# Performance work log

Hardware: AMD Instinct MI355X
Metric: run time of the kernel (lower is better)

Reference implementation:

```python
import jax, jax.numpy as jnp
import numpy as np

N = 100000   # nodes
E = 640000   # edges
G = 256      # graphs in batch
L = 3        # mpnn layers
D_IN = 64    # in_node_channels
E_IN = 16    # in_edge_channels
H = 128      # hidden width (uniform)


def setup_inputs() -> dict:
    key = jax.random.key(0)
    ks = jax.random.split(key, 20)
    s = 0.05
    inp = {
        "x": jax.random.normal(ks[0], (N, D_IN), dtype=jnp.float32),
        "edge_index": jax.random.randint(ks[1], (2, E), 0, N, dtype=jnp.int64),
        "edge_attr": jax.random.normal(ks[2], (E, E_IN), dtype=jnp.float32),
        "batch_vec": jnp.sort(jax.random.randint(ks[3], (N,), 0, G, dtype=jnp.int64)),
        # input encoders
        "Wn0": jax.random.normal(ks[4], (D_IN, H), dtype=jnp.float32) * s,
        "bn0": jnp.zeros((H,), jnp.float32),
        "We0": jax.random.normal(ks[5], (E_IN, H), dtype=jnp.float32) * s,
        "be0": jnp.zeros((H,), jnp.float32),
        # per-layer MPNN params (stacked over L)
        "WM": jax.random.normal(ks[6], (L, 3 * H, H), dtype=jnp.float32) * s,
        "bM": jnp.zeros((L, H), jnp.float32),
        "WU": jax.random.normal(ks[7], (L, 2 * H, H), dtype=jnp.float32) * s,
        "bU": jnp.zeros((L, H), jnp.float32),
        # per-layer node/edge linear layers
        "Wn": jax.random.normal(ks[8], (L, H, H), dtype=jnp.float32) * s,
        "bn": jnp.zeros((L, H), jnp.float32),
        "We": jax.random.normal(ks[9], (L, H, H), dtype=jnp.float32) * s,
        "be": jnp.zeros((L, H), jnp.float32),
        "Wh": jax.random.normal(ks[10], (H, 1), dtype=jnp.float32) * s,
        "bh": jnp.zeros((1,), jnp.float32),
    }
    return inp


def _mpnn_layer(x, edge_attr, src, dst, WM, bM, WU, bU):
    # message: relu(Linear([x_i, x_j, e]))  (x_i = target, x_j = source)
    xi = x[dst]                                   # [E, H]
    xj = x[src]                                   # [E, H]
    m = jax.nn.relu(jnp.concatenate([xi, xj, edge_attr], axis=-1) @ WM + bM)
    # mean aggregation at target nodes
    agg = jax.ops.segment_sum(m, dst, num_segments=N)        # [N, H]
    cnt = jax.ops.segment_sum(jnp.ones((m.shape[0], 1), x.dtype), dst,
                              num_segments=N)
    agg = agg / jnp.maximum(cnt, 1.0)
    # update: relu(Linear([x, aggr_out]))
    return jax.nn.relu(jnp.concatenate([x, agg], axis=-1) @ WU + bU)


def reference(x, edge_index, edge_attr, batch_vec,
              Wn0, bn0, We0, be0, WM, bM, WU, bU, Wn, bn, We, be, Wh, bh):
    src, dst = edge_index[0], edge_index[1]       # PyG source_to_target flow
    h = jax.nn.relu(x @ Wn0 + bn0)                # NodeFeatureLinear
    e = jax.nn.relu(edge_attr @ We0 + be0)        # EdgeFeatureLinear
    for i in range(L):
        h = _mpnn_layer(h, e, src, dst, WM[i], bM[i], WU[i], bU[i])
        h = jax.nn.relu(h @ Wn[i] + bn[i])
        e = jax.nn.relu(e @ We[i] + be[i])
    # global mean pool over graphs
    sums = jax.ops.segment_sum(h, batch_vec, num_segments=G)  # [G, H]
    cnts = jax.ops.segment_sum(jnp.ones((N, 1), h.dtype), batch_vec,
                               num_segments=G)
    pooled = sums / jnp.maximum(cnts, 1.0)
    return pooled @ Wh + bh                       # [G, 1]
```

## Files before the change

### kernel.cpp

```cpp
#include <hip/hip_runtime.h>

#define NN 100000
#define EE 640000
#define GG 256
#define LL 3
#define HH 128

constexpr int BM = 64;
constexpr int BK = 16;

typedef _Float16 f16;
typedef f16 f16x8 __attribute__((ext_vector_type(8)));
typedef f16 f16x4 __attribute__((ext_vector_type(4)));
typedef f16 f16x2 __attribute__((ext_vector_type(2)));
typedef float f32x4 __attribute__((ext_vector_type(4)));

#define TSTR 136

__device__ __forceinline__ void gload_lds16(const void* g, void* l) {
  __builtin_amdgcn_global_load_lds(
      (const __attribute__((address_space(1))) void*)g,
      (__attribute__((address_space(3))) void*)l, 16, 0, 0);
}

__global__ void prep_w(const float* __restrict__ We0,
                       const float* __restrict__ We,
                       const float* __restrict__ WM,
                       const float* __restrict__ Wn0,
                       const float* __restrict__ Wn,
                       const float* __restrict__ WU, f16* __restrict__ out) {
  const int buf = blockIdx.x >> 3;
  const int rowg = blockIdx.x & 7;
  const float* src;
  int K;
  if (buf == 0) {
    src = We0; K = 16;
  } else if (buf <= 2) {
    src = We + (size_t)(buf - 1) * HH * HH; K = HH;
  } else if (buf <= 5) {
    src = WM + (size_t)(buf - 3) * 3 * HH * HH + 2 * HH * HH; K = HH;
  } else if (buf == 6) {
    src = Wn0; K = 64;
  } else if (buf <= 9) {
    src = WM + (size_t)(buf - 7) * 3 * HH * HH; K = HH;
  } else if (buf <= 12) {
    src = WM + (size_t)(buf - 10) * 3 * HH * HH + HH * HH; K = HH;
  } else if (buf <= 15) {
    src = Wn + (size_t)(buf - 13) * HH * HH; K = HH;
  } else {
    const int t = buf - 16;
    src = WU + (size_t)(t >> 1) * 2 * HH * HH + (size_t)(t & 1) * HH * HH;
    K = HH;
  }
  f16* dst = out + (size_t)buf * HH * TSTR;
  for (int idx = threadIdx.x; idx < 16 * TSTR; idx += 256) {
    const int n = rowg * 16 + idx / TSTR;
    const int k = idx % TSTR;
    const float v = (k < K) ? src[(size_t)k * HH + n] : 0.f;
    dst[(size_t)n * TSTR + k] = (f16)v;
  }
}

struct GemmCtx {
  f16* Xs; f16* Wt; float* V;
  int tid, lane, wv, l15, q, m0;
};

__device__ __forceinline__ void ctx_init(GemmCtx& c, char* smem) {
  c.Xs = (f16*)smem;
  c.Wt = (f16*)(smem + 17408);
  c.V = (float*)(smem + 17408);
  c.tid = threadIdx.x;
  c.lane = c.tid & 63;
  c.wv = c.tid >> 6;
  c.l15 = c.lane & 15;
  c.q = c.lane >> 4;
  c.m0 = blockIdx.x * 64;
}

__device__ __forceinline__ void c_stageW(GemmCtx& c, const f16* Wg) {
  const char* g = (const char*)Wg;
  char* l = (char*)c.Wt;
#pragma unroll
  for (int i = 0; i < 8; ++i)
    gload_lds16(g + c.tid * 16 + i * 4096, l + c.tid * 16 + i * 4096);
  if (c.tid < 128) gload_lds16(g + c.tid * 16 + 32768, l + c.tid * 16 + 32768);
}

__device__ __forceinline__ void c_stageXf32(GemmCtx& c, const float* Xp,
                                            int stride, int KC, bool scale,
                                            const float* inv, int M) {
  const int npr = KC >> 2;
  for (int i = c.tid; i < 64 * npr; i += 256) {
    const int row = i / npr;
    const int c4 = (i - row * npr) << 2;
    float4 v = make_float4(0.f, 0.f, 0.f, 0.f);
    if (c.m0 + row < M) {
      v = *(const float4*)(Xp + (size_t)(c.m0 + row) * stride + c4);
      if (scale) {
        const float s = inv[c.m0 + row];
        v.x *= s; v.y *= s; v.z *= s; v.w *= s;
      }
    }
    f16x4 hv;
    hv[0] = (f16)v.x; hv[1] = (f16)v.y; hv[2] = (f16)v.z; hv[3] = (f16)v.w;
    *(f16x4*)&c.Xs[(size_t)row * TSTR + c4] = hv;
  }
}

__device__ __forceinline__ void c_stageX16(GemmCtx& c, const f16* Xp, int M) {
  for (int i = c.tid; i < 1024; i += 256) {
    const int row = i >> 4;
    const int c8 = (i & 15) << 3;
    f16x8 v = {};
    if (c.m0 + row < M) v = *(const f16x8*)(Xp + (size_t)(c.m0 + row) * HH + c8);
    *(f16x8*)&c.Xs[(size_t)row * TSTR + c8] = v;
  }
}

__device__ __forceinline__ void c_mfmaN(GemmCtx& c, f32x4 (&ac)[4][2],
                                        int nk) {
  for (int kk = 0; kk < nk; ++kk) {
    f16x8 a[4], b[2];
#pragma unroll
    for (int mi = 0; mi < 4; ++mi)
      a[mi] = *(const f16x8*)&c.Xs[(size_t)(mi * 16 + c.l15) * TSTR + kk * 32 +
                                   c.q * 8];
#pragma unroll
    for (int ni = 0; ni < 2; ++ni)
      b[ni] = *(const f16x8*)&c.Wt[(size_t)((c.wv * 2 + ni) * 16 + c.l15) *
                                       TSTR +
                                   kk * 32 + c.q * 8];
#pragma unroll
    for (int mi = 0; mi < 4; ++mi)
#pragma unroll
      for (int ni = 0; ni < 2; ++ni)
        ac[mi][ni] = __builtin_amdgcn_mfma_f32_16x16x32_f16(a[mi], b[ni],
                                                            ac[mi][ni], 0, 0,
                                                            0);
  }
}

__device__ __forceinline__ void c_zero(f32x4 (&ac)[4][2]) {
#pragma unroll
  for (int mi = 0; mi < 4; ++mi)
#pragma unroll
    for (int ni = 0; ni < 2; ++ni) {
      f32x4 z = {};
      ac[mi][ni] = z;
    }
}

__device__ __forceinline__ void c_reluXs(GemmCtx& c, f32x4 (&ac)[4][2],
                                         const float* bias) {
  const float bv0 = bias[c.wv * 32 + c.l15];
  const float bv1 = bias[c.wv * 32 + 16 + c.l15];
#pragma unroll
  for (int mi = 0; mi < 4; ++mi)
#pragma unroll
    for (int ni = 0; ni < 2; ++ni) {
      const float bb = ni ? bv1 : bv0;
#pragma unroll
      for (int rr = 0; rr < 4; ++rr) {
        float v = ac[mi][ni][rr] + bb;
        v = v > 0.f ? v : 0.f;
        c.Xs[(size_t)(mi * 16 + c.q * 4 + rr) * TSTR + c.wv * 32 + ni * 16 +
             c.l15] = (f16)v;
      }
    }
}

__device__ __forceinline__ void c_dumpV(GemmCtx& c, f32x4 (&ac)[4][2]) {
#pragma unroll
  for (int mi = 0; mi < 4; ++mi)
#pragma unroll
    for (int ni = 0; ni < 2; ++ni)
#pragma unroll
      for (int rr = 0; rr < 4; ++rr)
        c.V[(size_t)(mi * 16 + c.q * 4 + rr) * 132 + c.wv * 32 + ni * 16 +
            c.l15] = ac[mi][ni][rr];
}

__device__ __forceinline__ void c_storeV16(GemmCtx& c, f16* op, int M) {
  const int tm = (c.tid >> 4) << 2;
  const int tn = (c.tid & 15) << 3;
#pragma unroll
  for (int i = 0; i < 4; ++i) {
    const int r = c.m0 + tm + i;
    if (r >= M) continue;
    const float* vp = &c.V[(size_t)(tm + i) * 132 + tn];
    f16x8 hv;
#pragma unroll
    for (int j = 0; j < 8; ++j) hv[j] = (f16)vp[j];
    *(f16x8*)(op + (size_t)r * HH + tn) = hv;
  }
}

__device__ __forceinline__ void c_storeXs16(GemmCtx& c, f16* op, int M) {
  const int tm = (c.tid >> 4) << 2;
  const int tn = (c.tid & 15) << 3;
#pragma unroll
  for (int i = 0; i < 4; ++i) {
    const int r = c.m0 + tm + i;
    if (r >= M) continue;
    *(f16x8*)(op + (size_t)r * HH + tn) =
        *(const f16x8*)&c.Xs[(size_t)(tm + i) * TSTR + tn];
  }
}

__device__ __forceinline__ void c_projAB(GemmCtx& c, f32x4 (&ac)[4][2],
                                         const f16* WA, const f16* WBp,
                                         f16* A16, f16* B16, int M) {
  c_zero(ac);
  c_mfmaN(c, ac, 4);
  __syncthreads();
  c_dumpV(c, ac);
  __syncthreads();
  c_storeV16(c, A16, M);
  __syncthreads();
  c_stageW(c, WBp);
  __syncthreads();
  c_zero(ac);
  c_mfmaN(c, ac, 4);
  __syncthreads();
  c_dumpV(c, ac);
  __syncthreads();
  c_storeV16(c, B16, M);
}

__global__ __launch_bounds__(256) void fused_enc(
    const float* __restrict__ x, const f16* __restrict__ Wn0T,
    const float* __restrict__ bn0, f16* __restrict__ h16,
    const f16* __restrict__ WA, const f16* __restrict__ WBp,
    f16* __restrict__ A16, f16* __restrict__ B16, int M) {
  __shared__ __align__(16) char smem[17408 + 34816];
  GemmCtx c; ctx_init(c, smem);
  f32x4 acc[4][2];
  c_zero(acc);
  c_stageW(c, Wn0T);
  c_stageXf32(c, x, 64, 64, false, nullptr, M);
  __syncthreads();
  c_mfmaN(c, acc, 2);
  __syncthreads();
  c_reluXs(c, acc, bn0);
  c_stageW(c, WA);
  __syncthreads();
  c_storeXs16(c, h16, M);
  c_projAB(c, acc, WA, WBp, A16, B16, M);
}

template <int HAS_AB>
__global__ __launch_bounds__(256) void fused_upd(
    const f16* __restrict__ h, const f16* __restrict__ WU01,
    const float* __restrict__ bU, const float* __restrict__ agg,
    const float* __restrict__ invc, const f16* __restrict__ WnT,
    const float* __restrict__ bn, const f16* __restrict__ WA,
    const f16* __restrict__ WBp, f16* __restrict__ hout,
    f16* __restrict__ A16, f16* __restrict__ B16, int M) {
  __shared__ __align__(16) char smem[17408 + 34816];
  GemmCtx c; ctx_init(c, smem);
  f32x4 acc[4][2];
  c_zero(acc);
  c_stageW(c, WU01);
  c_stageX16(c, h, M);
  __syncthreads();
  c_mfmaN(c, acc, 4);
  __syncthreads();
  c_stageW(c, WU01 + (size_t)HH * TSTR);
  c_stageXf32(c, agg, HH, 128, true, invc, M);
  __syncthreads();
  c_mfmaN(c, acc, 4);
  __syncthreads();
  c_reluXs(c, acc, bU);
  c_stageW(c, WnT);
  __syncthreads();
  c_zero(acc);
  c_mfmaN(c, acc, 4);
  __syncthreads();
  c_reluXs(c, acc, bn);
  if (HAS_AB) c_stageW(c, WA);
  __syncthreads();
  c_storeXs16(c, hout, M);
  if (HAS_AB) c_projAB(c, acc, WA, WBp, A16, B16, M);
}

template <int CHAIN>
__global__ __launch_bounds__(512) void msg_k(
    const float* __restrict__ ea, const f16* __restrict__ W0T,
    const float* __restrict__ be0, const f16* __restrict__ WeT,
    const float* __restrict__ beL, const f16* __restrict__ WMeT,
    const float* __restrict__ bMl, const f16* __restrict__ A,
    const f16* __restrict__ B, const int* __restrict__ sIdx,
    const int* __restrict__ sSrc, const int* __restrict__ sDst,
    float* __restrict__ agg) {
  __shared__ __align__(16) char smem[34816 + 34816 + 512];
  f16* Tc = (f16*)smem;
  f16* Wc = (f16*)(smem + 34816);
  float* V = (float*)smem;
  int* dstS = (int*)(smem + 69632);

  const int tid = threadIdx.x;
  const int lane = tid & 63;
  const int wv = tid >> 6;
  const int ew = (wv >> 2) * 64;
  const int wn = wv & 3;
  const int l15 = lane & 15;
  const int q = lane >> 4;
  const int r0 = blockIdx.x * 128;

  auto wptr = [&](int p) -> const f16* {
    if (p == 0) return W0T;
    if (p <= CHAIN) return WeT + (size_t)(p - 1) * HH * TSTR;
    return WMeT;
  };

  auto stage_w = [&](const f16* Wg) {
    const char* g = (const char*)Wg;
    char* l = (char*)Wc;
#pragma unroll
    for (int i = 0; i < 4; ++i)
      gload_lds16(g + tid * 16 + i * 8192, l + tid * 16 + i * 8192);
    if (tid < 128) gload_lds16(g + tid * 16 + 32768, l + tid * 16 + 32768);
  };

  stage_w(wptr(0));
  {
    const int xr = tid >> 2;
    const int xc = (tid & 3) << 2;
    const int e = sIdx[r0 + xr];
    const float4 v = *(const float4*)(ea + (size_t)e * 16 + xc);
    f16x4 hv;
    hv[0] = (f16)v.x; hv[1] = (f16)v.y; hv[2] = (f16)v.z; hv[3] = (f16)v.w;
    *(f16x4*)&Tc[(size_t)xr * TSTR + xc] = hv;
    f16x4 z = {};
    *(f16x4*)&Tc[(size_t)xr * TSTR + 16 + xc] = z;
    if (tid < 128) dstS[tid] = sDst[r0 + tid];
  }

  f32x4 acc[4][2];

  auto zero_acc = [&]() {
#pragma unroll
    for (int mi = 0; mi < 4; ++mi)
#pragma unroll
      for (int ni = 0; ni < 2; ++ni) {
        f32x4 z = {};
        acc[mi][ni] = z;
      }
  };

  auto mfma_steps = [&](int nk) {
    for (int kk = 0; kk < nk; ++kk) {
      f16x8 a[4], b[2];
#pragma unroll
      for (int mi = 0; mi < 4; ++mi)
        a[mi] = *(const f16x8*)&Tc[(size_t)(ew + mi * 16 + l15) * TSTR +
                                   kk * 32 + q * 8];
#pragma unroll
      for (int ni = 0; ni < 2; ++ni)
        b[ni] = *(const f16x8*)&Wc[(size_t)((wn * 2 + ni) * 16 + l15) * TSTR +
                                   kk * 32 + q * 8];
#pragma unroll
      for (int mi = 0; mi < 4; ++mi)
#pragma unroll
        for (int ni = 0; ni < 2; ++ni)
          acc[mi][ni] = __builtin_amdgcn_mfma_f32_16x16x32_f16(
              a[mi], b[ni], acc[mi][ni], 0, 0, 0);
    }
  };

  auto relu_body = [&](const float* bias) {
    float bv0 = bias[wn * 32 + l15];
    float bv1 = bias[wn * 32 + 16 + l15];
#pragma unroll
    for (int mi = 0; mi < 4; ++mi)
#pragma unroll
      for (int ni = 0; ni < 2; ++ni) {
        const float bb = ni ? bv1 : bv0;
#pragma unroll
        for (int rr = 0; rr < 4; ++rr) {
          float v = acc[mi][ni][rr] + bb;
          v = v > 0.f ? v : 0.f;
          Tc[(size_t)(ew + mi * 16 + q * 4 + rr) * TSTR + wn * 32 + ni * 16 +
             l15] = (f16)v;
        }
      }
  };

  zero_acc();
  __syncthreads();
  mfma_steps(1);
  __syncthreads();
  stage_w(wptr(1));
  relu_body(be0);
  __syncthreads();

#pragma unroll
  for (int s = 0; s < CHAIN; ++s) {
    zero_acc();
    mfma_steps(4);
    __syncthreads();
    stage_w(wptr(s + 2));
    relu_body(beL + (size_t)s * HH);
    __syncthreads();
  }

  zero_acc();
  mfma_steps(4);
  __syncthreads();

#pragma unroll
  for (int mi = 0; mi < 4; ++mi)
#pragma unroll
    for (int ni = 0; ni < 2; ++ni)
#pragma unroll
      for (int rr = 0; rr < 4; ++rr)
        V[(size_t)(ew + mi * 16 + q * 4 + rr) * 129 + wn * 32 + ni * 16 +
          l15] = acc[mi][ni][rr];
  __syncthreads();

  const int tm = (tid >> 4) << 2;
  const int tn = (tid & 15) << 3;
  const float4 m0v = *(const float4*)(bMl + tn);
  const float4 m1v = *(const float4*)(bMl + tn + 4);
  const float mv[8] = {m0v.x, m0v.y, m0v.z, m0v.w,
                       m1v.x, m1v.y, m1v.z, m1v.w};
#pragma unroll
  for (int i = 0; i < 4; ++i) {
    const int rr = r0 + tm + i;
    const int d = dstS[tm + i];
    const int s = sSrc[rr];
    const f16x8 a8 = *(const f16x8*)(A + (size_t)d * HH + tn);
    const f16x8 b8 = *(const f16x8*)(B + (size_t)s * HH + tn);
    float* vp = &V[(size_t)(tm + i) * 129 + tn];
#pragma unroll
    for (int j = 0; j < 8; ++j)
      vp[j] = fmaxf(vp[j] + (float)a8[j] + (float)b8[j] + mv[j], 0.f);
  }
  __syncthreads();

  const int c = tid & 127;
  const int h = tid >> 7;
  float racc = 0.f;
  int cur = dstS[h * 32];
  bool first = true;
  for (int e2 = h * 32; e2 < h * 32 + 32; ++e2) {
    const int d = dstS[e2];
    if (d != cur) {
      if (first) {
        atomicAdd(&agg[(size_t)cur * HH + c], racc);
        first = false;
      } else {
        agg[(size_t)cur * HH + c] = racc;
      }
      racc = 0.f;
      cur = d;
    }
    racc += V[(size_t)e2 * 129 + c];
  }
  atomicAdd(&agg[(size_t)cur * HH + c], racc);
}

__global__ void count_kernel(const int* __restrict__ dst, int* cnt, int E) {
  const int i = blockIdx.x * 256 + threadIdx.x;
  if (i < E) atomicAdd(&cnt[dst[i]], 1);
}

__global__ void invcnt_kernel(const int* __restrict__ cnt, float* inv, int n) {
  const int i = blockIdx.x * 256 + threadIdx.x;
  if (i < n) inv[i] = 1.0f / (float)max(cnt[i], 1);
}

__global__ void scan_block(const int* __restrict__ cnt, int* excl, int* bsum,
                           int n) {
  __shared__ int s[256];
  const int tx = threadIdx.x;
  const int i = blockIdx.x * 256 + tx;
  const int v = (i < n) ? cnt[i] : 0;
  s[tx] = v;
  __syncthreads();
  for (int off = 1; off < 256; off <<= 1) {
    int tv = (tx >= off) ? s[tx - off] : 0;
    __syncthreads();
    s[tx] += tv;
    __syncthreads();
  }
  if (i < n) excl[i] = s[tx] - v;
  if (tx == 255) bsum[blockIdx.x] = s[255];
}

__global__ __launch_bounds__(512) void scan_bsum(int* bsum, int nb) {
  __shared__ int s[512];
  const int t = threadIdx.x;
  const int v0 = (t < nb) ? bsum[t] : 0;
  s[t] = v0;
  __syncthreads();
  for (int off = 1; off < 512; off <<= 1) {
    const int tv = (t >= off) ? s[t - off] : 0;
    __syncthreads();
    s[t] += tv;
    __syncthreads();
  }
  if (t < nb) bsum[t] = s[t] - v0;
}

__global__ void scan_add(int* excl, const int* __restrict__ bsum, int n) {
  const int i = blockIdx.x * 256 + threadIdx.x;
  if (i < n) excl[i] += bsum[blockIdx.x];
}

__global__ void scatter_edges(const int* __restrict__ dst,
                              const int* __restrict__ src,
                              const int* __restrict__ off, int* ctr, int* sIdx,
                              int* sSrc, int* sDst, int E) {
  const int e = blockIdx.x * 256 + threadIdx.x;
  if (e >= E) return;
  const int d = dst[e];
  const int p = off[d] + atomicAdd(&ctr[d], 1);
  sIdx[p] = e;
  sSrc[p] = src[e];
  sDst[p] = d;
}

__global__ void pool_accum(const f16* __restrict__ h,
                           const int* __restrict__ batch,
                           float* __restrict__ gsum, int M) {
  const int col = threadIdx.x;
  const int r0 = blockIdx.x * 64;
  const int rend = min(r0 + 64, M);
  if (r0 >= M) return;
  float acc = 0.f;
  int cur = batch[r0];
  for (int r = r0; r < rend; ++r) {
    const int b = batch[r];
    if (b != cur) {
      atomicAdd(&gsum[(size_t)cur * HH + col], acc);
      acc = 0.f;
      cur = b;
    }
    acc += (float)h[(size_t)r * HH + col];
  }
  atomicAdd(&gsum[(size_t)cur * HH + col], acc);
}

__global__ void gcnt_kernel(const int* __restrict__ batch, int* gcnt, int n) {
  const int i = blockIdx.x * 256 + threadIdx.x;
  if (i < n) atomicAdd(&gcnt[batch[i]], 1);
}

__global__ void head_kernel(const float* __restrict__ gsum,
                            const int* __restrict__ gcnt,
                            const float* __restrict__ Wh,
                            const float* __restrict__ bh,
                            float* __restrict__ out) {
  const int g = blockIdx.x;
  const int t = threadIdx.x;
  float v = gsum[(size_t)g * HH + t] * Wh[t];
#pragma unroll
  for (int o = 32; o > 0; o >>= 1) v += __shfl_down(v, o, 64);
  __shared__ float red[2];
  if ((t & 63) == 0) red[t >> 6] = v;
  __syncthreads();
  if (t == 0) {
    const float s = red[0] + red[1];
    const float c = (float)max(gcnt[g], 1);
    out[g] = s / c + bh[0];
  }
}

extern "C" void kernel_launch(void* const* d_in, const int* in_sizes, int n_in,
                              void* d_out, int out_size, void* d_ws,
                              size_t ws_size, hipStream_t stream) {
  (void)in_sizes; (void)n_in; (void)out_size;
  const float* x = (const float*)d_in[0];
  const int* ei = (const int*)d_in[1];
  const float* ea = (const float*)d_in[2];
  const int* batch = (const int*)d_in[3];
  const float* Wn0 = (const float*)d_in[4];
  const float* bn0 = (const float*)d_in[5];
  const float* We0 = (const float*)d_in[6];
  const float* be0 = (const float*)d_in[7];
  const float* WM = (const float*)d_in[8];
  const float* bM = (const float*)d_in[9];
  const float* WU = (const float*)d_in[10];
  const float* bU = (const float*)d_in[11];
  const float* Wn = (const float*)d_in[12];
  const float* bn = (const float*)d_in[13];
  const float* We = (const float*)d_in[14];
  const float* be = (const float*)d_in[15];
  const float* Wh = (const float*)d_in[16];
  const float* bh = (const float*)d_in[17];

  const int* srcI = ei;
  const int* dstI = ei + EE;

  float* w = (float*)d_ws;
  size_t o = 0;
  f16* h16 = (f16*)(w + o);  o += (size_t)NN * HH / 2;
  float* agg = w + o;  o += (size_t)NN * HH;
  f16* A16 = (f16*)(w + o); o += (size_t)NN * HH / 2;
  f16* B16 = (f16*)(w + o); o += (size_t)NN * HH / 2;
  float* gsum = w + o; o += (size_t)GG * HH;
  float* invc = w + o; o += (size_t)NN;
  int* cnt = (int*)(w + o);  o += (size_t)NN;
  int* gcnt = (int*)(w + o); o += (size_t)GG;
  int* off = (int*)(w + o);  o += (size_t)NN;
  int* ctr = (int*)(w + o);  o += (size_t)NN;
  int* bsum = (int*)(w + o); o += 512;
  int* sIdx = (int*)(w + o); o += (size_t)EE;
  int* sSrc = (int*)(w + o); o += (size_t)EE;
  int* sDst = (int*)(w + o); o += (size_t)EE;
  f16* Wp = (f16*)(w + o);   o += (size_t)22 * HH * TSTR / 2;
  if (o * sizeof(float) > ws_size) return;

  auto WB = [&](int i) { return Wp + (size_t)i * HH * TSTR; };

  const dim3 blk(256);
  const int gridN = (NN + BM - 1) / BM;
  const int gridE = EE / 128;
  const int NBLK = (NN + 255) / 256;

  hipMemsetAsync(cnt, 0, (size_t)NN * sizeof(int), stream);
  hipMemsetAsync(ctr, 0, (size_t)NN * sizeof(int), stream);
  hipMemsetAsync(gsum, 0, (size_t)GG * HH * sizeof(float), stream);
  hipMemsetAsync(gcnt, 0, (size_t)GG * sizeof(int), stream);

  count_kernel<<<(EE + 255) / 256, blk, 0, stream>>>(dstI, cnt, EE);
  scan_block<<<NBLK, blk, 0, stream>>>(cnt, off, bsum, NN);
  scan_bsum<<<1, dim3(512), 0, stream>>>(bsum, NBLK);
  scan_add<<<NBLK, blk, 0, stream>>>(off, bsum, NN);
  scatter_edges<<<(EE + 255) / 256, blk, 0, stream>>>(dstI, srcI, off, ctr,
                                                      sIdx, sSrc, sDst, EE);
  invcnt_kernel<<<(NN + 255) / 256, blk, 0, stream>>>(cnt, invc, NN);
  prep_w<<<22 * 8, blk, 0, stream>>>(We0, We, WM, Wn0, Wn, WU, Wp);

  fused_enc<<<gridN, blk, 0, stream>>>(x, WB(6), bn0, h16, WB(7), WB(10),
                                       A16, B16, NN);

  for (int l = 0; l < LL; ++l) {
    hipMemsetAsync(agg, 0, (size_t)NN * HH * sizeof(float), stream);
    switch (l) {
      case 0:
        msg_k<0><<<gridE, dim3(512), 0, stream>>>(
            ea, WB(0), be0, WB(1), be, WB(3), bM + 0 * HH, A16, B16, sIdx,
            sSrc, sDst, agg);
        break;
      case 1:
        msg_k<1><<<gridE, dim3(512), 0, stream>>>(
            ea, WB(0), be0, WB(1), be, WB(4), bM + 1 * HH, A16, B16, sIdx,
            sSrc, sDst, agg);
        break;
      default:
        msg_k<2><<<gridE, dim3(512), 0, stream>>>(
            ea, WB(0), be0, WB(1), be, WB(5), bM + 2 * HH, A16, B16, sIdx,
            sSrc, sDst, agg);
        break;
    }
    if (l < LL - 1) {
      fused_upd<1><<<gridN, blk, 0, stream>>>(
          h16, WB(16 + 2 * l), bU + l * HH, agg, invc, WB(13 + l), bn + l * HH,
          WB(7 + l + 1), WB(10 + l + 1), h16, A16, B16, NN);
    } else {
      fused_upd<0><<<gridN, blk, 0, stream>>>(
          h16, WB(16 + 2 * l), bU + l * HH, agg, invc, WB(13 + l), bn + l * HH,
          nullptr, nullptr, h16, nullptr, nullptr, NN);
    }
  }

  pool_accum<<<gridN, dim3(128), 0, stream>>>(h16, batch, gsum, NN);
  gcnt_kernel<<<(NN + 255) / 256, blk, 0, stream>>>(batch, gcnt, NN);
  head_kernel<<<GG, dim3(128), 0, stream>>>(gsum, gcnt, Wh, bh, (float*)d_out);
}
```

Baseline: 985.2 us.

## Fuse pooling into last update, shrink message kernel to 256 threads with f16 staging

The final update kernel now accumulates the global mean-pool sums directly from its LDS tile, so the separate pool_accum and gcnt kernels go away. gcnt counting moves into count_kernel and the inverse-count computation into scan_add, which removes two more launches. The message kernel now runs 256 threads per block, each wave covering a 64x64 output tile with 16 accumulators. Its message buffer is staged as f16 instead of f32, halving LDS traffic at the cost of extra rounding before aggregation, and the larger per-wave tile raises register pressure.

```diff
diff --git a/kernel.cpp b/kernel.cpp
--- a/kernel.cpp
+++ b/kernel.cpp
@@ -7,7 +7,6 @@
 #define HH 128
 
 constexpr int BM = 64;
-constexpr int BK = 16;
 
 typedef _Float16 f16;
 typedef f16 f16x8 __attribute__((ext_vector_type(8)));
@@ -256,9 +255,13 @@
     const float* __restrict__ invc, const f16* __restrict__ WnT,
     const float* __restrict__ bn, const f16* __restrict__ WA,
     const f16* __restrict__ WBp, f16* __restrict__ hout,
-    f16* __restrict__ A16, f16* __restrict__ B16, int M) {
+    f16* __restrict__ A16, f16* __restrict__ B16,
+    const int* __restrict__ batch, float* __restrict__ gsum, int M) {
   __shared__ __align__(16) char smem[17408 + 34816];
+  __shared__ int bat[64];
   GemmCtx c; ctx_init(c, smem);
+  if (!HAS_AB && c.tid < 64 && c.m0 + c.tid < M)
+    bat[c.tid] = batch[c.m0 + c.tid];
   f32x4 acc[4][2];
   c_zero(acc);
   c_stageW(c, WU01);
@@ -280,12 +283,33 @@
   c_reluXs(c, acc, bn);
   if (HAS_AB) c_stageW(c, WA);
   __syncthreads();
-  c_storeXs16(c, hout, M);
-  if (HAS_AB) c_projAB(c, acc, WA, WBp, A16, B16, M);
+  if (HAS_AB) {
+    c_storeXs16(c, hout, M);
+    c_projAB(c, acc, WA, WBp, A16, B16, M);
+  } else {
+    const int col = c.tid & 127;
+    const int rg = c.tid >> 7;
+    const int lo = rg * 32;
+    const int hi = min(lo + 32, M - c.m0);
+    if (lo < hi) {
+      float a2 = 0.f;
+      int cur = bat[lo];
+      for (int r = lo; r < hi; ++r) {
+        const int b = bat[r];
+        if (b != cur) {
+          atomicAdd(&gsum[(size_t)cur * HH + col], a2);
+          a2 = 0.f;
+          cur = b;
+        }
+        a2 += (float)c.Xs[(size_t)r * TSTR + col];
+      }
+      atomicAdd(&gsum[(size_t)cur * HH + col], a2);
+    }
+  }
 }
 
 template <int CHAIN>
-__global__ __launch_bounds__(512) void msg_k(
+__global__ __launch_bounds__(256) void msg_k(
     const float* __restrict__ ea, const f16* __restrict__ W0T,
     const float* __restrict__ be0, const f16* __restrict__ WeT,
     const float* __restrict__ beL, const f16* __restrict__ WMeT,
@@ -296,14 +320,14 @@
   __shared__ __align__(16) char smem[34816 + 34816 + 512];
   f16* Tc = (f16*)smem;
   f16* Wc = (f16*)(smem + 34816);
-  float* V = (float*)smem;
+  f16* V16 = (f16*)smem;
   int* dstS = (int*)(smem + 69632);
 
   const int tid = threadIdx.x;
   const int lane = tid & 63;
   const int wv = tid >> 6;
-  const int ew = (wv >> 2) * 64;
-  const int wn = wv & 3;
+  const int eh = (wv >> 1) * 64;
+  const int ch = wv & 1;
   const int l15 = lane & 15;
   const int q = lane >> 4;
   const int r0 = blockIdx.x * 128;
@@ -318,32 +342,34 @@
     const char* g = (const char*)Wg;
     char* l = (char*)Wc;
 #pragma unroll
-    for (int i = 0; i < 4; ++i)
-      gload_lds16(g + tid * 16 + i * 8192, l + tid * 16 + i * 8192);
+    for (int i = 0; i < 8; ++i)
+      gload_lds16(g + tid * 16 + i * 4096, l + tid * 16 + i * 4096);
     if (tid < 128) gload_lds16(g + tid * 16 + 32768, l + tid * 16 + 32768);
   };
 
   stage_w(wptr(0));
   {
-    const int xr = tid >> 2;
-    const int xc = (tid & 3) << 2;
+    const int xr = tid >> 1;
+    const int hf = (tid & 1) << 3;
     const int e = sIdx[r0 + xr];
-    const float4 v = *(const float4*)(ea + (size_t)e * 16 + xc);
-    f16x4 hv;
-    hv[0] = (f16)v.x; hv[1] = (f16)v.y; hv[2] = (f16)v.z; hv[3] = (f16)v.w;
-    *(f16x4*)&Tc[(size_t)xr * TSTR + xc] = hv;
-    f16x4 z = {};
-    *(f16x4*)&Tc[(size_t)xr * TSTR + 16 + xc] = z;
+    const float4 v0 = *(const float4*)(ea + (size_t)e * 16 + hf);
+    const float4 v1 = *(const float4*)(ea + (size_t)e * 16 + hf + 4);
+    f16x8 hv;
+    hv[0] = (f16)v0.x; hv[1] = (f16)v0.y; hv[2] = (f16)v0.z; hv[3] = (f16)v0.w;
+    hv[4] = (f16)v1.x; hv[5] = (f16)v1.y; hv[6] = (f16)v1.z; hv[7] = (f16)v1.w;
+    *(f16x8*)&Tc[(size_t)xr * TSTR + hf] = hv;
+    f16x8 z = {};
+    *(f16x8*)&Tc[(size_t)xr * TSTR + 16 + hf] = z;
     if (tid < 128) dstS[tid] = sDst[r0 + tid];
   }
 
-  f32x4 acc[4][2];
+  f32x4 acc[4][4];
 
   auto zero_acc = [&]() {
 #pragma unroll
     for (int mi = 0; mi < 4; ++mi)
 #pragma unroll
-      for (int ni = 0; ni < 2; ++ni) {
+      for (int ni = 0; ni < 4; ++ni) {
         f32x4 z = {};
         acc[mi][ni] = z;
       }
@@ -351,37 +377,35 @@
 
   auto mfma_steps = [&](int nk) {
     for (int kk = 0; kk < nk; ++kk) {
-      f16x8 a[4], b[2];
+      f16x8 a[4], b[4];
 #pragma unroll
       for (int mi = 0; mi < 4; ++mi)
-        a[mi] = *(const f16x8*)&Tc[(size_t)(ew + mi * 16 + l15) * TSTR +
+        a[mi] = *(const f16x8*)&Tc[(size_t)(eh + mi * 16 + l15) * TSTR +
                                    kk * 32 + q * 8];
 #pragma unroll
-      for (int ni = 0; ni < 2; ++ni)
-        b[ni] = *(const f16x8*)&Wc[(size_t)((wn * 2 + ni) * 16 + l15) * TSTR +
+      for (int ni = 0; ni < 4; ++ni)
+        b[ni] = *(const f16x8*)&Wc[(size_t)((ch * 4 + ni) * 16 + l15) * TSTR +
                                    kk * 32 + q * 8];
 #pragma unroll
       for (int mi = 0; mi < 4; ++mi)
 #pragma unroll
-        for (int ni = 0; ni < 2; ++ni)
+        for (int ni = 0; ni < 4; ++ni)
           acc[mi][ni] = __builtin_amdgcn_mfma_f32_16x16x32_f16(
               a[mi], b[ni], acc[mi][ni], 0, 0, 0);
     }
   };
 
   auto relu_body = [&](const float* bias) {
-    float bv0 = bias[wn * 32 + l15];
-    float bv1 = bias[wn * 32 + 16 + l15];
 #pragma unroll
     for (int mi = 0; mi < 4; ++mi)
 #pragma unroll
-      for (int ni = 0; ni < 2; ++ni) {
-        const float bb = ni ? bv1 : bv0;
+      for (int ni = 0; ni < 4; ++ni) {
+        const float bb = bias[ch * 64 + ni * 16 + l15];
 #pragma unroll
         for (int rr = 0; rr < 4; ++rr) {
           float v = acc[mi][ni][rr] + bb;
           v = v > 0.f ? v : 0.f;
-          Tc[(size_t)(ew + mi * 16 + q * 4 + rr) * TSTR + wn * 32 + ni * 16 +
+          Tc[(size_t)(eh + mi * 16 + q * 4 + rr) * TSTR + ch * 64 + ni * 16 +
              l15] = (f16)v;
         }
       }
@@ -412,63 +436,66 @@
 #pragma unroll
   for (int mi = 0; mi < 4; ++mi)
 #pragma unroll
-    for (int ni = 0; ni < 2; ++ni)
+    for (int ni = 0; ni < 4; ++ni)
 #pragma unroll
       for (int rr = 0; rr < 4; ++rr)
-        V[(size_t)(ew + mi * 16 + q * 4 + rr) * 129 + wn * 32 + ni * 16 +
-          l15] = acc[mi][ni][rr];
-  __syncthreads();
-
-  const int tm = (tid >> 4) << 2;
+        V16[(size_t)(eh + mi * 16 + q * 4 + rr) * TSTR + ch * 64 + ni * 16 +
+            l15] = (f16)acc[mi][ni][rr];
+  __syncthreads();
+
+  const int rg = tid >> 4;
   const int tn = (tid & 15) << 3;
   const float4 m0v = *(const float4*)(bMl + tn);
   const float4 m1v = *(const float4*)(bMl + tn + 4);
   const float mv[8] = {m0v.x, m0v.y, m0v.z, m0v.w,
                        m1v.x, m1v.y, m1v.z, m1v.w};
 #pragma unroll
-  for (int i = 0; i < 4; ++i) {
-    const int rr = r0 + tm + i;
-    const int d = dstS[tm + i];
+  for (int i = 0; i < 8; ++i) {
+    const int row = rg * 8 + i;
+    const int rr = r0 + row;
+    const int d = dstS[row];
     const int s = sSrc[rr];
     const f16x8 a8 = *(const f16x8*)(A + (size_t)d * HH + tn);
     const f16x8 b8 = *(const f16x8*)(B + (size_t)s * HH + tn);
-    float* vp = &V[(size_t)(tm + i) * 129 + tn];
+    f16* vp = &V16[(size_t)row * TSTR + tn];
+    const f16x8 pv = *(const f16x8*)vp;
+    f16x8 o;
 #pragma unroll
     for (int j = 0; j < 8; ++j)
-      vp[j] = fmaxf(vp[j] + (float)a8[j] + (float)b8[j] + mv[j], 0.f);
+      o[j] = (f16)fmaxf((float)pv[j] + (float)a8[j] + (float)b8[j] + mv[j],
+                        0.f);
+    *(f16x8*)vp = o;
   }
   __syncthreads();
 
   const int c = tid & 127;
-  const int h = tid >> 7;
-  float racc = 0.f;
-  int cur = dstS[h * 32];
-  bool first = true;
-  for (int e2 = h * 32; e2 < h * 32 + 32; ++e2) {
-    const int d = dstS[e2];
-    if (d != cur) {
-      if (first) {
-        atomicAdd(&agg[(size_t)cur * HH + c], racc);
-        first = false;
-      } else {
-        agg[(size_t)cur * HH + c] = racc;
+  for (int sp = tid >> 7; sp < 4; sp += 2) {
+    float racc = 0.f;
+    int cur = dstS[sp * 32];
+    bool first = true;
+    for (int e2 = sp * 32; e2 < sp * 32 + 32; ++e2) {
+      const int d = dstS[e2];
+      if (d != cur) {
+        if (first) {
+          atomicAdd(&agg[(size_t)cur * HH + c], racc);
+          first = false;
+        } else {
+          agg[(size_t)cur * HH + c] = racc;
+        }
+        racc = 0.f;
+        cur = d;
       }
-      racc = 0.f;
-      cur = d;
-    }
-    racc += V[(size_t)e2 * 129 + c];
-  }
-  atomicAdd(&agg[(size_t)cur * HH + c], racc);
-}
-
-__global__ void count_kernel(const int* __restrict__ dst, int* cnt, int E) {
+      racc += (float)V16[(size_t)e2 * TSTR + c];
+    }
+    atomicAdd(&agg[(size_t)cur * HH + c], racc);
+  }
+}
+
+__global__ void count_kernel(const int* __restrict__ dst, int* cnt,
+                             const int* __restrict__ batch, int* gcnt) {
   const int i = blockIdx.x * 256 + threadIdx.x;
-  if (i < E) atomicAdd(&cnt[dst[i]], 1);
-}
-
-__global__ void invcnt_kernel(const int* __restrict__ cnt, float* inv, int n) {
-  const int i = blockIdx.x * 256 + threadIdx.x;
-  if (i < n) inv[i] = 1.0f / (float)max(cnt[i], 1);
+  if (i < EE) atomicAdd(&cnt[dst[i]], 1);
+  if (i < NN) atomicAdd(&gcnt[batch[i]], 1);
 }
 
 __global__ void scan_block(const int* __restrict__ cnt, int* excl, int* bsum,
@@ -504,9 +531,14 @@
   if (t < nb) bsum[t] = s[t] - v0;
 }
 
-__global__ void scan_add(int* excl, const int* __restrict__ bsum, int n) {
+__global__ void scan_add(int* excl, const int* __restrict__ bsum,
+                         const int* __restrict__ cnt, float* __restrict__ inv,
+                         int n) {
   const int i = blockIdx.x * 256 + threadIdx.x;
-  if (i < n) excl[i] += bsum[blockIdx.x];
+  if (i < n) {
+    excl[i] += bsum[blockIdx.x];
+    inv[i] = 1.0f / (float)max(cnt[i], 1);
+  }
 }
 
 __global__ void scatter_edges(const int* __restrict__ dst,
@@ -520,32 +552,6 @@
   sIdx[p] = e;
   sSrc[p] = src[e];
   sDst[p] = d;
-}
-
-__global__ void pool_accum(const f16* __restrict__ h,
-                           const int* __restrict__ batch,
-                           float* __restrict__ gsum, int M) {
-  const int col = threadIdx.x;
-  const int r0 = blockIdx.x * 64;
-  const int rend = min(r0 + 64, M);
-  if (r0 >= M) return;
-  float acc = 0.f;
-  int cur = batch[r0];
-  for (int r = r0; r < rend; ++r) {
-    const int b = batch[r];
-    if (b != cur) {
-      atomicAdd(&gsum[(size_t)cur * HH + col], acc);
-      acc = 0.f;
-      cur = b;
-    }
-    acc += (float)h[(size_t)r * HH + col];
-  }
-  atomicAdd(&gsum[(size_t)cur * HH + col], acc);
-}
-
-__global__ void gcnt_kernel(const int* __restrict__ batch, int* gcnt, int n) {
-  const int i = blockIdx.x * 256 + threadIdx.x;
-  if (i < n) atomicAdd(&gcnt[batch[i]], 1);
 }
 
 __global__ void head_kernel(const float* __restrict__ gsum,
@@ -625,13 +631,12 @@
   hipMemsetAsync(gsum, 0, (size_t)GG * HH * sizeof(float), stream);
   hipMemsetAsync(gcnt, 0, (size_t)GG * sizeof(int), stream);
 
-  count_kernel<<<(EE + 255) / 256, blk, 0, stream>>>(dstI, cnt, EE);
+  count_kernel<<<(EE + 255) / 256, blk, 0, stream>>>(dstI, cnt, batch, gcnt);
   scan_block<<<NBLK, blk, 0, stream>>>(cnt, off, bsum, NN);
   scan_bsum<<<1, dim3(512), 0, stream>>>(bsum, NBLK);
-  scan_add<<<NBLK, blk, 0, stream>>>(off, bsum, NN);
+  scan_add<<<NBLK, blk, 0, stream>>>(off, bsum, cnt, invc, NN);
   scatter_edges<<<(EE + 255) / 256, blk, 0, stream>>>(dstI, srcI, off, ctr,
                                                       sIdx, sSrc, sDst, EE);
-  invcnt_kernel<<<(NN + 255) / 256, blk, 0, stream>>>(cnt, invc, NN);
   prep_w<<<22 * 8, blk, 0, stream>>>(We0, We, WM, Wn0, Wn, WU, Wp);
 
   fused_enc<<<gridN, blk, 0, stream>>>(x, WB(6), bn0, h16, WB(7), WB(10),
@@ -641,33 +646,31 @@
     hipMemsetAsync(agg, 0, (size_t)NN * HH * sizeof(float), stream);
     switch (l) {
       case 0:
-        msg_k<0><<<gridE, dim3(512), 0, stream>>>(
-            ea, WB(0), be0, WB(1), be, WB(3), bM + 0 * HH, A16, B16, sIdx,
-            sSrc, sDst, agg);
+        msg_k<0><<<gridE, blk, 0, stream>>>(ea, WB(0), be0, WB(1), be, WB(3),
+                                            bM + 0 * HH, A16, B16, sIdx, sSrc,
+                                            sDst, agg);
         break;
       case 1:
-        msg_k<1><<<gridE, dim3(512), 0, stream>>>(
-            ea, WB(0), be0, WB(1), be, WB(4), bM + 1 * HH, A16, B16, sIdx,
-            sSrc, sDst, agg);
+        msg_k<1><<<gridE, blk, 0, stream>>>(ea, WB(0), be0, WB(1), be, WB(4),
+                                            bM + 1 * HH, A16, B16, sIdx, sSrc,
+                                            sDst, agg);
         break;
       default:
-        msg_k<2><<<gridE, dim3(512), 0, stream>>>(
-            ea, WB(0), be0, WB(1), be, WB(5), bM + 2 * HH, A16, B16, sIdx,
-            sSrc, sDst, agg);
+        msg_k<2><<<gridE, blk, 0, stream>>>(ea, WB(0), be0, WB(1), be, WB(5),
+                                            bM + 2 * HH, A16, B16, sIdx, sSrc,
+                                            sDst, agg);
         break;
     }
     if (l < LL - 1) {
       fused_upd<1><<<gridN, blk, 0, stream>>>(
           h16, WB(16 + 2 * l), bU + l * HH, agg, invc, WB(13 + l), bn + l * HH,
-          WB(7 + l + 1), WB(10 + l + 1), h16, A16, B16, NN);
+          WB(7 + l + 1), WB(10 + l + 1), h16, A16, B16, nullptr, nullptr, NN);
     } else {
       fused_upd<0><<<gridN, blk, 0, stream>>>(
           h16, WB(16 + 2 * l), bU + l * HH, agg, invc, WB(13 + l), bn + l * HH,
-          nullptr, nullptr, h16, nullptr, nullptr, NN);
-    }
-  }
-
-  pool_accum<<<gridN, dim3(128), 0, stream>>>(h16, batch, gsum, NN);
-  gcnt_kernel<<<(NN + 255) / 256, blk, 0, stream>>>(batch, gcnt, NN);
+          nullptr, nullptr, nullptr, nullptr, nullptr, batch, gsum, NN);
+    }
+  }
+
   head_kernel<<<GG, dim3(128), 0, stream>>>(gsum, gcnt, Wh, bh, (float*)d_out);
 }
```

After: 1.055 ms. +7.1%, slower.
